# Kernel optimization log

Measured on AMD Instinct MI355X. Metric: run time of the kernel, lower is better.

The kernel has to match this reference:

```python
import jax, jax.numpy as jnp
import numpy as np

E = 8            # num experts
CAP_FACTOR = 1.5
K_THRESH = 0.8
BAL_ALPHA = 0.005
REG_ALPHA = 1e-6
BN_EPS = 1e-5
POOL = 16


def setup_inputs() -> dict:
    key = jax.random.key(0)
    ks = jax.random.split(key, 8)
    B, H, L, D = 128, 1024, 512, 1024
    return {
        "x": jax.random.normal(ks[0], (B, H, L), jnp.float32),
        "conv_w": jax.random.normal(ks[1], (64, H, 3), jnp.float32) / np.float32(np.sqrt(3 * H)),
        "conv_b": jnp.zeros((64,), jnp.float32),
        "bn_gamma": jnp.ones((64 * POOL,), jnp.float32),
        "bn_beta": jnp.zeros((64 * POOL,), jnp.float32),
        "fc1_w": jax.random.normal(ks[2], (128, 64 * POOL), jnp.float32) / np.float32(np.sqrt(64 * POOL)),
        "fc1_b": jnp.zeros((128,), jnp.float32),
        "fc2_w": jax.random.normal(ks[3], (E, 128), jnp.float32) / np.float32(np.sqrt(128)),
        "fc2_b": jnp.zeros((E,), jnp.float32),
        "exp_w": jax.random.normal(ks[4], (E, H, D), jnp.float32) / np.float32(np.sqrt(H)),
        "exp_b": jnp.zeros((E, D), jnp.float32),
    }


def _forward(x, conv_w, conv_b, bn_gamma, bn_beta, fc1_w, fc1_b, fc2_w, fc2_b, exp_w, exp_b):
    B, H, L = x.shape
    # ---- router: Conv1d(H->64,k=3,p=1) -> GELU -> AdaptiveAvgPool1d(16) -> Flatten -> BN -> FC -> GELU -> FC -> softmax
    h = jax.lax.conv_general_dilated(x, conv_w, (1,), ((1, 1),),
                                     dimension_numbers=("NCH", "OIH", "NCH"))
    h = jax.nn.gelu(h + conv_b[None, :, None], approximate=False)          # [B,64,L]; torch GELU is exact erf
    h = h.reshape(B, 64, POOL, L // POOL).mean(-1).reshape(B, 64 * POOL)   # adaptive avg pool (L%16==0) + flatten
    mu, var = h.mean(0), h.var(0)                                          # training-mode (Sync)BatchNorm: batch stats
    h = (h - mu) / jnp.sqrt(var + BN_EPS) * bn_gamma + bn_beta
    h = jax.nn.gelu(h @ fc1_w.T + fc1_b, approximate=False)
    rw = jax.nn.softmax(h @ fc2_w.T + fc2_b, axis=1)                       # [B,E]; expert dropout = identity (eval)
    # ---- dynamic k: smallest k s.t. cumsum of sorted probs > threshold; only max over batch is used
    topk_w, topk_idx = jax.lax.top_k(rw, E)                                # full descending sort
    cum = jnp.cumsum(topk_w, axis=1)
    over = cum > K_THRESH
    k_per = jnp.where(jnp.any(over, axis=1), jnp.argmax(over, axis=1) + 1, E)
    max_k = jnp.max(jnp.clip(k_per, 1, E))
    col_valid = jnp.arange(E)[None, :] < max_k                             # broadcast [B,E]; cols >= max_k unused
    assign = jnp.where(col_valid, topk_idx, -1)
    # ---- capacity enforcement: per expert keep the `capacity` highest-weight assignments, drop the rest (-1)
    capacity = max(1, int(B * CAP_FACTOR / E))
    flat_idx, flat_w = assign.reshape(-1), topk_w.reshape(-1)              # row-major [B*E], matches torch flatten

    def keep_for_expert(e):
        m = flat_idx == e
        order = jnp.argsort(-jnp.where(m, flat_w, -jnp.inf))               # descending within expert e
        ranks = jnp.zeros_like(order).at[order].set(jnp.arange(order.shape[0]))
        return m & (ranks < capacity)

    keep = jax.vmap(keep_for_expert)(jnp.arange(E))                        # [E, B*E]
    counts = keep.sum(axis=1).astype(jnp.float32)                          # == bincount of valid final indices
    final_idx = jnp.where(jnp.any(keep, axis=0), flat_idx, -1).reshape(B, E)
    # ---- experts: mean-pool over length, per-expert Linear(H->D); gather each sample's selected experts
    pooled = x.mean(axis=2)                                                # [B,H]
    y = jnp.einsum("bh,ehd->bed", pooled, exp_w) + exp_b[None]             # [B,E,D] all-expert outputs
    outputs = jnp.take_along_axis(y, jnp.clip(final_idx, 0)[..., None], axis=1)
    outputs = jnp.where(final_idx[..., None] >= 0, outputs, 0.0)           # dropped slots contribute zeros
    # ---- combine: softmax over the max_k slots; dropped (-1) slots enter softmax with logit 0, as in torch
    logits = jnp.where(col_valid, topk_w * (final_idx >= 0), -jnp.inf)
    norm_w = jax.nn.softmax(logits, axis=1)                                # [B,E]
    pooler = jnp.einsum("bkd,bk->bd", outputs, norm_w)                     # [B,D]
    # ---- losses / stats
    usage = rw.mean(0)
    reg = jnp.sum(exp_w * exp_w) + jnp.sum(exp_b * exp_b)                  # sum ||param||_2^2 over expert params
    added_loss = BAL_ALPHA * jnp.var(usage, ddof=1) + REG_ALPHA * reg      # torch.var is unbiased
    return pooler, added_loss, usage, counts


def reference(x, conv_w, conv_b, bn_gamma, bn_beta, fc1_w, fc1_b, fc2_w, fc2_b, exp_w, exp_b):
    return _forward(x, conv_w, conv_b, bn_gamma, bn_beta, fc1_w, fc1_b, fc2_w, fc2_b, exp_w, exp_b)
```

## Files before the change

### kernel.cpp

```cpp
#include <hip/hip_runtime.h>
#include <hip/hip_bf16.h>
#include <math.h>

#define NB 128
#define NH 1024
#define NL 512
#define OC 64
#define NE 8
#define ND 1024
#define CAPACITY 24

static const size_t WS_PART  = 0;
static const size_t WS_WSEP  = 1048576;
static const size_t WS_PXT   = 2097152;
static const size_t WS_HPOOL = 2228224;
static const size_t WS_SCALE = 2359296;
static const size_t WS_SHIFT = 2360320;
static const size_t WS_A1    = 2361344;
static const size_t WS_TKW   = 2377728;
static const size_t WS_TKI   = 2378752;
static const size_t WS_USAGE = 2379784;
static const size_t WS_VARU  = 2379792;
static const size_t WS_REG   = 2379793;
static const size_t WS_CNT   = 2379794;
static const size_t WS_WMAT  = 2380832;
static const size_t WS_RW    = 2381856;
static const size_t WS_KP    = 2382880;

typedef __attribute__((ext_vector_type(8))) short bf16x8;
typedef __attribute__((ext_vector_type(4))) float f32x4;

__device__ __forceinline__ float gelu_exact(float v) {
    return 0.5f * v * (1.0f + erff(v * 0.70710678118654752440f));
}

__device__ __forceinline__ unsigned short f2bf_rne(float f) {
    unsigned int u = __float_as_uint(f);
    unsigned int r = u + 0x7FFFu + ((u >> 16) & 1u);
    return (unsigned short)(r >> 16);
}
__device__ __forceinline__ float bf2f(unsigned short h) {
    return __uint_as_float(((unsigned int)h) << 16);
}

__device__ __forceinline__ unsigned cvtpk_bf16(float a, float b) {
    unsigned r;
    asm("v_cvt_pk_bf16_f32 %0, %1, %2" : "=v"(r) : "v"(a), "v"(b));
    return r;
}

__global__ __launch_bounds__(256) void k_wsplit(const float* __restrict__ cw, float* __restrict__ ws)
{
    if (blockIdx.x == 0 && threadIdx.x == 0) ws[WS_REG] = 0.0f;
    unsigned short* wsep = (unsigned short*)(ws + WS_WSEP);
    int i = blockIdx.x * 256 + threadIdx.x;
    float v = cw[i];
    int j = i % 3;
    int t = i / 3;
    int h = t & 1023;
    int o = t >> 10;
    int it = h >> 5;
    int h5 = h & 31;
    int e = h5 & 7;
    int lane = (o & 15) | ((h5 >> 3) << 4);
    int mt = (o >> 4) & 3;
    unsigned short hi = f2bf_rne(v);
    unsigned short lo = f2bf_rne(v - bf2f(hi));
    size_t base = ((size_t)((it * 3 + j) * 4 + mt) * 2) * 512 + lane * 8 + e;
    wsep[base] = hi;
    wsep[base + 512] = lo;
}

__device__ __forceinline__ void cvt_unit(unsigned int* X, int lq, int h4,
                                         const float4* v, float* sh)
{
    sh[0] = sh[1] = sh[2] = sh[3] = 0.f;
#pragma unroll
    for (int i = 0; i < 4; ++i) {
        float a0 = ((const float*)&v[0])[i];
        float a1 = ((const float*)&v[1])[i];
        float a2 = ((const float*)&v[2])[i];
        float a3 = ((const float*)&v[3])[i];
        sh[0] += a0; sh[1] += a1; sh[2] += a2; sh[3] += a3;
        unsigned h01 = cvtpk_bf16(a0, a1);
        unsigned h23 = cvtpk_bf16(a2, a3);
        float r0 = a0 - __uint_as_float(h01 << 16);
        float r1 = a1 - __uint_as_float(h01 & 0xFFFF0000u);
        float r2 = a2 - __uint_as_float(h23 << 16);
        float r3 = a3 - __uint_as_float(h23 & 0xFFFF0000u);
        unsigned l01 = cvtpk_bf16(r0, r1);
        unsigned l23 = cvtpk_bf16(r2, r3);
        int r = lq * 4 + i;
        unsigned int* dst = X + r * 34 + ((2 * h4) ^ ((r & 3) << 2));
        *(uint2*)dst = make_uint2(h01, h23);
        *(uint2*)(dst + 16) = make_uint2(l01, l23);
    }
}

__global__ __launch_bounds__(256, 2) void k_convmfma(const float* __restrict__ x,
                                                     const float* __restrict__ cb,
                                                     float* __restrict__ ws)
{
    __shared__ unsigned int Xb[2][136 * 34];
    __shared__ float xs2[3][128];
    __shared__ float scb[64];

    const int lc = blockIdx.x, b = blockIdx.y;
    const int l0 = lc * 128;
    const int tid = threadIdx.x;
    const int wv = tid >> 6, lane = tid & 63;
    const int h4 = tid & 7;
    const int lqi = 1 + (tid >> 3);
    const bool has_halo = (tid < 16);
    const int lqh = (tid < 8) ? 0 : 33;
    const bool halo_ok = (tid < 8) ? (lc > 0) : (lc < 3);

    const unsigned short* wsg = (const unsigned short*)(ws + WS_WSEP);
    const float* xbase = x + (size_t)b * (NH * NL);
    float* poolp = ws + WS_PART + ((size_t)(lc * 128 + b)) * 1024;

    if (tid < 64) scb[tid] = cb[tid];

    f32x4 acc[4][2];
#pragma unroll
    for (int mt = 0; mt < 4; ++mt)
#pragma unroll
        for (int nt = 0; nt < 2; ++nt) acc[mt][nt] = (f32x4){0.f, 0.f, 0.f, 0.f};

    float4 xA[4], hA[4], xB[4], hB[4];

    auto xload = [&](int itL, float4* xc, float4* hc) {
        const int hn = itL * 32;
        const float* p = xbase + (size_t)(hn + h4 * 4) * NL + (l0 - 4 + lqi * 4);
#pragma unroll
        for (int jj = 0; jj < 4; ++jj) xc[jj] = *(const float4*)(p + jj * NL);
        if (has_halo) {
            int gl = l0 - 4 + lqh * 4;
#pragma unroll
            for (int jj = 0; jj < 4; ++jj)
                hc[jj] = halo_ok ? *(const float4*)(xbase + (size_t)(hn + h4 * 4 + jj) * NL + gl)
                                 : make_float4(0.f, 0.f, 0.f, 0.f);
        }
    };

    auto body = [&](int it, float4* xc, float4* hc) {
        unsigned int* Xw = Xb[it & 1];
        bf16x8 Ar[3][4][2];
        {
            const unsigned short* abase = wsg + (size_t)it * 12288 + lane * 8;
#pragma unroll
            for (int j = 0; j < 3; ++j)
#pragma unroll
                for (int mt = 0; mt < 4; ++mt) {
                    Ar[j][mt][0] = *(const bf16x8*)(abase + (size_t)(j * 8 + mt * 2) * 512);
                    Ar[j][mt][1] = *(const bf16x8*)(abase + (size_t)(j * 8 + mt * 2 + 1) * 512);
                }
        }
        {
            float sh[4];
            cvt_unit(Xw, lqi, h4, xc, sh);
#pragma unroll
            for (int jj = 0; jj < 4; ++jj) {
                float s = sh[jj];
                s += __shfl_xor(s, 8, 64);
                s += __shfl_xor(s, 16, 64);
                s += __shfl_xor(s, 32, 64);
                if ((lane >> 3) == 0) xs2[it % 3][wv * 32 + h4 * 4 + jj] = s;
            }
            if (has_halo) { float d[4]; cvt_unit(Xw, lqh, h4, hc, d); }
        }
        __syncthreads();
        if (it > 0 && tid < 32) {
            const float* S = xs2[(it - 1) % 3];
            poolp[(it - 1) * 32 + tid] = S[tid] + S[32 + tid] + S[64 + tid] + S[96 + tid];
        }
        if (it < 30) xload(it + 2, xc, hc);
        const int g4 = (lane >> 4) << 2;
#pragma unroll
        for (int j = 0; j < 3; ++j) {
            bf16x8 Bh[2], Bl[2];
#pragma unroll
            for (int nt = 0; nt < 2; ++nt) {
                int rx = 3 + j + wv * 32 + nt * 16 + (lane & 15);
                const unsigned int* bp = Xw + rx * 34 + (g4 ^ ((rx & 3) << 2));
                Bh[nt] = *(const bf16x8*)bp;
                Bl[nt] = *(const bf16x8*)(bp + 16);
            }
#pragma unroll
            for (int mt = 0; mt < 4; ++mt)
#pragma unroll
                for (int nt = 0; nt < 2; ++nt) {
                    acc[mt][nt] = __builtin_amdgcn_mfma_f32_16x16x32_bf16(Ar[j][mt][0], Bh[nt], acc[mt][nt], 0, 0, 0);
                    acc[mt][nt] = __builtin_amdgcn_mfma_f32_16x16x32_bf16(Ar[j][mt][0], Bl[nt], acc[mt][nt], 0, 0, 0);
                    acc[mt][nt] = __builtin_amdgcn_mfma_f32_16x16x32_bf16(Ar[j][mt][1], Bh[nt], acc[mt][nt], 0, 0, 0);
                }
        }
    };

    xload(0, xA, hA);
    xload(1, xB, hB);

    for (int it2 = 0; it2 < 32; it2 += 2) {
        body(it2, xA, hA);
        body(it2 + 1, xB, hB);
    }
    if (tid < 32) {
        const float* S = xs2[31 % 3];
        poolp[31 * 32 + tid] = S[tid] + S[32 + tid] + S[64 + tid] + S[96 + tid];
    }

    {
        const int g = lane >> 4, cidx = lane & 15;
#pragma unroll
        for (int mt = 0; mt < 4; ++mt) {
            float s[4];
#pragma unroll
            for (int r = 0; r < 4; ++r) {
                int o = mt * 16 + g * 4 + r;
                float bo = scb[o];
                s[r] = gelu_exact(acc[mt][0][r] + bo) + gelu_exact(acc[mt][1][r] + bo);
            }
#pragma unroll
            for (int m = 1; m < 16; m <<= 1) {
#pragma unroll
                for (int r = 0; r < 4; ++r) s[r] += __shfl_xor(s[r], m, 64);
            }
            if (cidx == 0) {
#pragma unroll
                for (int r = 0; r < 4; ++r) {
                    int o = mt * 16 + g * 4 + r;
                    ws[WS_HPOOL + (size_t)b * 1024 + o * 16 + lc * 4 + wv] = s[r] * (1.0f / 32.0f);
                }
            }
        }
    }
}

__global__ __launch_bounds__(256) void k_mid(const float* __restrict__ g,
                                             const float* __restrict__ bet,
                                             float* __restrict__ ws)
{
    int bx = blockIdx.x;
    if (bx < 512) {
        int id = bx * 256 + threadIdx.x;
        int b = id >> 10, h = id & 1023;
        float s = 0.0f;
#pragma unroll
        for (int lcc = 0; lcc < 4; lcc++) s += ws[WS_PART + ((size_t)(lcc * 128 + b)) * 1024 + h];
        ws[WS_PXT + (size_t)h * 128 + b] = s * (1.0f / 512.0f);
    } else {
        int f = (bx - 512) * 256 + threadIdx.x;
        const float* hp = ws + WS_HPOOL;
        float s = 0.0f;
        for (int b = 0; b < 128; b++) s += hp[(size_t)b * 1024 + f];
        float mu = s * (1.0f / 128.0f);
        float v = 0.0f;
        for (int b = 0; b < 128; b++) { float d = hp[(size_t)b * 1024 + f] - mu; v += d * d; }
        float var = v * (1.0f / 128.0f);
        float sc = g[f] / sqrtf(var + 1e-5f);
        ws[WS_SCALE + f] = sc;
        ws[WS_SHIFT + f] = bet[f] - mu * sc;
    }
}

__global__ __launch_bounds__(256) void k_fused(const float* __restrict__ w1,
                                               const float* __restrict__ b1,
                                               const float* __restrict__ w2,
                                               const float* __restrict__ b2,
                                               const float* __restrict__ ew,
                                               const float* __restrict__ eb,
                                               float* __restrict__ ws)
{
    __shared__ float smem[6400];
    const int bx = blockIdx.x;
    const int tid = threadIdx.x;

    if (bx < 256) {
        float* a_s = smem;
        float* b_s = smem + 4096;
        float* red2 = smem + 6144;
        const int e = bx >> 5, dt = (bx >> 1) & 15, ks = bx & 1;
        const int tb = tid >> 3, td = tid & 7;
        float acc[4][8];
#pragma unroll
        for (int i = 0; i < 4; i++)
#pragma unroll
            for (int j = 0; j < 8; j++) acc[i][j] = 0.0f;
        float ssq = 0.0f;

        const float* pxt = ws + WS_PXT;
        for (int kt = 0; kt < 512; kt += 32) {
            __syncthreads();
            for (int idx = tid; idx < 4096; idx += 256) {
                int kk = idx >> 7, bb = idx & 127;
                a_s[kk * 128 + bb] = pxt[(size_t)(ks * 512 + kt + kk) * 128 + bb];
            }
            for (int idx = tid; idx < 2048; idx += 256) {
                int kk = idx >> 6, d = idx & 63;
                float v = ew[(size_t)e * 1048576 + (size_t)(ks * 512 + kt + kk) * 1024 + dt * 64 + d];
                b_s[kk * 64 + d] = v;
                ssq += v * v;
            }
            __syncthreads();
#pragma unroll 4
            for (int kk = 0; kk < 32; kk++) {
                float4 av = *(const float4*)&a_s[kk * 128 + tb * 4];
                float4 b0 = *(const float4*)&b_s[kk * 64 + td * 8];
                float4 b1v = *(const float4*)&b_s[kk * 64 + td * 8 + 4];
                float aa[4] = {av.x, av.y, av.z, av.w};
                float bb4[8] = {b0.x, b0.y, b0.z, b0.w, b1v.x, b1v.y, b1v.z, b1v.w};
#pragma unroll
                for (int i = 0; i < 4; i++)
#pragma unroll
                    for (int j = 0; j < 8; j++) acc[i][j] = fmaf(aa[i], bb4[j], acc[i][j]);
            }
        }
        float* outp = ws + WS_PART + ((size_t)(ks * 8 + e) * 128) * 1024 + dt * 64;
#pragma unroll
        for (int i = 0; i < 4; i++) {
            int bb = tb * 4 + i;
            *(float4*)(outp + (size_t)bb * 1024 + td * 8) =
                make_float4(acc[i][0], acc[i][1], acc[i][2], acc[i][3]);
            *(float4*)(outp + (size_t)bb * 1024 + td * 8 + 4) =
                make_float4(acc[i][4], acc[i][5], acc[i][6], acc[i][7]);
        }
        if (bx == 0)
            for (int i = tid; i < 8192; i += 256) { float v = eb[i]; ssq += v * v; }
        red2[tid] = ssq;
        __syncthreads();
        for (int off = 128; off > 0; off >>= 1) {
            if (tid < off) red2[tid] += red2[tid + off];
            __syncthreads();
        }
        if (tid == 0) atomicAdd(ws + WS_REG, red2[0]);
    } else {
        float* hb  = smem;
        float* red = smem + 1024;
        float* ha  = smem + 1280;
        float* w2s = smem + 1408;
        float* lg  = smem + 2432;
        const int b = bx - 256;
        const float* hp = ws + WS_HPOOL + (size_t)b * 1024;
        for (int k = tid; k < 1024; k += 256)
            hb[k] = hp[k] * ws[WS_SCALE + k] + ws[WS_SHIFT + k];
        for (int i = tid; i < 1024; i += 256) w2s[i] = w2[i];
        __syncthreads();
        int o = tid & 127, kh = tid >> 7;
        const float4* wrp = (const float4*)(w1 + (size_t)o * 1024 + kh * 512);
        const float* hx = hb + kh * 512;
        float acc = 0.0f;
#pragma unroll 4
        for (int k = 0; k < 128; k++) {
            float4 w = wrp[k];
            acc = fmaf(hx[4 * k], w.x, acc);     acc = fmaf(hx[4 * k + 1], w.y, acc);
            acc = fmaf(hx[4 * k + 2], w.z, acc); acc = fmaf(hx[4 * k + 3], w.w, acc);
        }
        red[tid] = acc;
        __syncthreads();
        if (tid < 128)
            ha[tid] = gelu_exact(red[tid] + red[tid + 128] + b1[tid]);
        __syncthreads();
        if (tid < 8) {
            float a2 = b2[tid];
            for (int k = 0; k < 128; k++) a2 = fmaf(ha[k], w2s[tid * 128 + k], a2);
            lg[tid] = a2;
        }
        __syncthreads();
        if (tid == 0) {
            float rw[8];
            float m = -1e30f;
#pragma unroll
            for (int e = 0; e < 8; e++) m = fmaxf(m, lg[e]);
            float s = 0.0f;
#pragma unroll
            for (int e = 0; e < 8; e++) { rw[e] = expf(lg[e] - m); s += rw[e]; }
            float inv = 1.0f / s;
#pragma unroll
            for (int e = 0; e < 8; e++) { rw[e] *= inv; ws[WS_RW + b * 8 + e] = rw[e]; }
            float tw[8]; int ti[8]; unsigned used = 0;
#pragma unroll
            for (int r = 0; r < 8; r++) {
                float bv = -1e30f; int bi = 0;
#pragma unroll
                for (int e = 0; e < 8; e++) {
                    bool take = !((used >> e) & 1u) && (rw[e] > bv);
                    bv = take ? rw[e] : bv;
                    bi = take ? e : bi;
                }
                used |= (1u << bi);
                tw[r] = bv; ti[r] = bi;
            }
            float cum = 0.0f; int kp = 8;
#pragma unroll
            for (int r = 0; r < 8; r++) {
                cum += tw[r];
                if (cum > 0.8f) { kp = r + 1; break; }
            }
#pragma unroll
            for (int r = 0; r < 8; r++) {
                ws[WS_TKW + b * 8 + r] = tw[r];
                ((int*)ws)[WS_TKI + b * 8 + r] = ti[r];
            }
            ((int*)ws)[WS_KP + b] = kp;
        }
    }
}

__global__ __launch_bounds__(128) void k_route(float* __restrict__ ws)
{
    __shared__ float tkw_s[1024];
    __shared__ int   tki_s[1024];
    __shared__ int   keep_s[1024];
    __shared__ float wv_s[128];
    __shared__ int   sv_s[128];
    __shared__ float usg[8];
    __shared__ int   cnt_s[8];
    __shared__ int   mk;

    const int tid = threadIdx.x;
    const int b = tid;
    if (tid == 0) mk = 0;
    if (tid < 8) cnt_s[tid] = 0;
    __syncthreads();
    atomicMax(&mk, ((const int*)ws)[WS_KP + b]);
#pragma unroll
    for (int r = 0; r < 8; r++) {
        tkw_s[b * 8 + r] = ws[WS_TKW + b * 8 + r];
        tki_s[b * 8 + r] = ((const int*)ws)[WS_TKI + b * 8 + r];
    }
    __syncthreads();
    const int maxk = mk;

    if (tid < 8) {
        float s2 = 0.0f;
        for (int bb = 0; bb < 128; bb++) s2 += ws[WS_RW + bb * 8 + tid];
        float u = s2 * (1.0f / 128.0f);
        usg[tid] = u;
        ws[WS_USAGE + tid] = u;
    }
    __syncthreads();
    if (tid == 0) {
        float mu = 0.0f;
#pragma unroll
        for (int e = 0; e < 8; e++) mu += usg[e];
        mu *= (1.0f / 8.0f);
        float v = 0.0f;
#pragma unroll
        for (int e = 0; e < 8; e++) { float d = usg[e] - mu; v += d * d; }
        ws[WS_VARU] = v * (1.0f / 7.0f);
    }

    for (int e = 0; e < 8; ++e) {
        float myw = 0.0f; int mys = -1;
        for (int k = 0; k < maxk; k++)
            if (tki_s[b * 8 + k] == e) { myw = tkw_s[b * 8 + k]; mys = b * 8 + k; }
        wv_s[b] = myw; sv_s[b] = mys;
        __syncthreads();
        if (mys >= 0) {
            int rank = 0;
            for (int b2 = 0; b2 < 128; b2++) {
                int s2 = sv_s[b2];
                if (s2 >= 0) {
                    float w2v = wv_s[b2];
                    if (w2v > myw || (w2v == myw && s2 < mys)) rank++;
                }
            }
            int kept = (rank < CAPACITY) ? 1 : 0;
            keep_s[mys] = kept;
            if (kept) atomicAdd(&cnt_s[e], 1);
        }
        __syncthreads();
    }
    if (tid < 8) ws[WS_CNT + tid] = (float)cnt_s[tid];

    float lv[8]; int kept[8]; int idx[8];
#pragma unroll
    for (int k = 0; k < 8; k++) {
        if (k < maxk) {
            kept[k] = keep_s[b * 8 + k];
            idx[k] = tki_s[b * 8 + k];
            lv[k] = kept[k] ? tkw_s[b * 8 + k] : 0.0f;
        } else { kept[k] = 0; idx[k] = -1; lv[k] = -1e30f; }
    }
    float mx = -1e30f;
#pragma unroll
    for (int k = 0; k < 8; k++) if (k < maxk) mx = fmaxf(mx, lv[k]);
    float s3 = 0.0f; float ev[8];
#pragma unroll
    for (int k = 0; k < 8; k++) { ev[k] = (k < maxk) ? expf(lv[k] - mx) : 0.0f; s3 += ev[k]; }
    float inv3 = 1.0f / s3;
    float Wr[8] = {0, 0, 0, 0, 0, 0, 0, 0};
#pragma unroll
    for (int k = 0; k < 8; k++) {
        if (kept[k]) {
            float v = ev[k] * inv3;
#pragma unroll
            for (int e = 0; e < 8; e++) Wr[e] += (idx[k] == e) ? v : 0.0f;
        }
    }
#pragma unroll
    for (int e = 0; e < 8; e++) ws[WS_WMAT + b * 8 + e] = Wr[e];
}

__global__ __launch_bounds__(256) void k_final(const float* __restrict__ eb,
                                               const float* __restrict__ ws,
                                               float* __restrict__ out)
{
    int id = blockIdx.x * 256 + threadIdx.x;
    int b = id >> 10, d = id & 1023;
    const float* wm = ws + WS_WMAT + b * 8;
    const float* Y = ws + WS_PART;
    float s = 0.0f;
#pragma unroll
    for (int e = 0; e < 8; e++) {
        float y = Y[((size_t)e * 128 + b) * 1024 + d]
                + Y[((size_t)(8 + e) * 128 + b) * 1024 + d]
                + eb[(size_t)e * 1024 + d];
        s += wm[e] * y;
    }
    out[id] = s;
    if (blockIdx.x == 0) {
        int t = threadIdx.x;
        if (t == 0) out[131072] = 0.005f * ws[WS_VARU] + 1e-6f * ws[WS_REG];
        else if (t >= 1 && t < 9)  out[131072 + t] = ws[WS_USAGE + t - 1];
        else if (t >= 9 && t < 17) out[131072 + t] = ws[WS_CNT + t - 9];
    }
}

extern "C" void kernel_launch(void* const* d_in, const int* in_sizes, int n_in,
                              void* d_out, int out_size, void* d_ws, size_t ws_size,
                              hipStream_t stream)
{
    const float* x   = (const float*)d_in[0];
    const float* cw  = (const float*)d_in[1];
    const float* cb  = (const float*)d_in[2];
    const float* bng = (const float*)d_in[3];
    const float* bnb = (const float*)d_in[4];
    const float* f1w = (const float*)d_in[5];
    const float* f1b = (const float*)d_in[6];
    const float* f2w = (const float*)d_in[7];
    const float* f2b = (const float*)d_in[8];
    const float* ew  = (const float*)d_in[9];
    const float* eb  = (const float*)d_in[10];
    float* ws  = (float*)d_ws;
    float* out = (float*)d_out;

    k_wsplit  <<<768, 256, 0, stream>>>(cw, ws);
    k_convmfma<<<dim3(4, 128), 256, 0, stream>>>(x, cb, ws);
    k_mid     <<<516, 256, 0, stream>>>(bng, bnb, ws);
    k_fused   <<<384, 256, 0, stream>>>(f1w, f1b, f2w, f2b, ew, eb, ws);
    k_route   <<<1, 128, 0, stream>>>(ws);
    k_final   <<<512, 256, 0, stream>>>(eb, ws, out);
}
```

Measured before the change: 316.0 us.

## Repartition conv MFMA by output-channel per wave, vectorize wsplit and final, finer expert tiles

The conv kernel now gives each wave one 16-channel M tile across all eight 16-column N tiles, instead of all four M tiles across two N tiles. That cuts per-wave A-fragment register loads from 24 to 6 and lowers register pressure, at the cost of more LDS B reads. The weight-split kernel now writes packed 16-byte vectors per thread, the expert GEMM uses 32-wide D tiles over twice as many blocks for better occupancy, and the final combine kernel is vectorized with float4. Together these change work partitioning and memory access patterns across several kernels.

```diff
diff --git a/kernel.cpp b/kernel.cpp
--- a/kernel.cpp
+++ b/kernel.cpp
@@ -16,7 +16,6 @@
 static const size_t WS_HPOOL = 2228224;
 static const size_t WS_SCALE = 2359296;
 static const size_t WS_SHIFT = 2360320;
-static const size_t WS_A1    = 2361344;
 static const size_t WS_TKW   = 2377728;
 static const size_t WS_TKI   = 2378752;
 static const size_t WS_USAGE = 2379784;
@@ -54,21 +53,22 @@
     if (blockIdx.x == 0 && threadIdx.x == 0) ws[WS_REG] = 0.0f;
     unsigned short* wsep = (unsigned short*)(ws + WS_WSEP);
     int i = blockIdx.x * 256 + threadIdx.x;
-    float v = cw[i];
-    int j = i % 3;
-    int t = i / 3;
-    int h = t & 1023;
-    int o = t >> 10;
-    int it = h >> 5;
-    int h5 = h & 31;
-    int e = h5 & 7;
-    int lane = (o & 15) | ((h5 >> 3) << 4);
-    int mt = (o >> 4) & 3;
-    unsigned short hi = f2bf_rne(v);
-    unsigned short lo = f2bf_rne(v - bf2f(hi));
-    size_t base = ((size_t)((it * 3 + j) * 4 + mt) * 2) * 512 + lane * 8 + e;
-    wsep[base] = hi;
-    wsep[base + 512] = lo;
+    int lane = i & 63;
+    int split = (i >> 6) & 1;
+    int mt = (i >> 7) & 3;
+    int rest = i >> 9;
+    int j = rest % 3;
+    int it = rest / 3;
+    int o = mt * 16 + (lane & 15);
+    int hb = it * 32 + ((lane >> 4) << 3);
+    unsigned short v8[8];
+#pragma unroll
+    for (int e = 0; e < 8; ++e) {
+        float v = cw[((size_t)o * 1024 + hb + e) * 3 + j];
+        unsigned short hi = f2bf_rne(v);
+        v8[e] = split ? f2bf_rne(v - bf2f(hi)) : hi;
+    }
+    *(uint4*)(wsep + ((size_t)((it * 3 + j) * 4 + mt) * 2 + split) * 512 + lane * 8) = *(uint4*)v8;
 }
 
 __device__ __forceinline__ void cvt_unit(unsigned int* X, int lq, int h4,
@@ -121,11 +121,9 @@
 
     if (tid < 64) scb[tid] = cb[tid];
 
-    f32x4 acc[4][2];
-#pragma unroll
-    for (int mt = 0; mt < 4; ++mt)
-#pragma unroll
-        for (int nt = 0; nt < 2; ++nt) acc[mt][nt] = (f32x4){0.f, 0.f, 0.f, 0.f};
+    f32x4 acc[8];
+#pragma unroll
+    for (int nt = 0; nt < 8; ++nt) acc[nt] = (f32x4){0.f, 0.f, 0.f, 0.f};
 
     float4 xA[4], hA[4], xB[4], hB[4];
 
@@ -145,16 +143,14 @@
 
     auto body = [&](int it, float4* xc, float4* hc) {
         unsigned int* Xw = Xb[it & 1];
-        bf16x8 Ar[3][4][2];
+        bf16x8 Ah[3], Al[3];
         {
             const unsigned short* abase = wsg + (size_t)it * 12288 + lane * 8;
 #pragma unroll
-            for (int j = 0; j < 3; ++j)
-#pragma unroll
-                for (int mt = 0; mt < 4; ++mt) {
-                    Ar[j][mt][0] = *(const bf16x8*)(abase + (size_t)(j * 8 + mt * 2) * 512);
-                    Ar[j][mt][1] = *(const bf16x8*)(abase + (size_t)(j * 8 + mt * 2 + 1) * 512);
-                }
+            for (int j = 0; j < 3; ++j) {
+                Ah[j] = *(const bf16x8*)(abase + (size_t)((j * 4 + wv) * 2) * 512);
+                Al[j] = *(const bf16x8*)(abase + (size_t)((j * 4 + wv) * 2 + 1) * 512);
+            }
         }
         {
             float sh[4];
@@ -178,22 +174,16 @@
         const int g4 = (lane >> 4) << 2;
 #pragma unroll
         for (int j = 0; j < 3; ++j) {
-            bf16x8 Bh[2], Bl[2];
-#pragma unroll
-            for (int nt = 0; nt < 2; ++nt) {
-                int rx = 3 + j + wv * 32 + nt * 16 + (lane & 15);
+#pragma unroll
+            for (int nt = 0; nt < 8; ++nt) {
+                int rx = 3 + j + nt * 16 + (lane & 15);
                 const unsigned int* bp = Xw + rx * 34 + (g4 ^ ((rx & 3) << 2));
-                Bh[nt] = *(const bf16x8*)bp;
-                Bl[nt] = *(const bf16x8*)(bp + 16);
-            }
-#pragma unroll
-            for (int mt = 0; mt < 4; ++mt)
-#pragma unroll
-                for (int nt = 0; nt < 2; ++nt) {
-                    acc[mt][nt] = __builtin_amdgcn_mfma_f32_16x16x32_bf16(Ar[j][mt][0], Bh[nt], acc[mt][nt], 0, 0, 0);
-                    acc[mt][nt] = __builtin_amdgcn_mfma_f32_16x16x32_bf16(Ar[j][mt][0], Bl[nt], acc[mt][nt], 0, 0, 0);
-                    acc[mt][nt] = __builtin_amdgcn_mfma_f32_16x16x32_bf16(Ar[j][mt][1], Bh[nt], acc[mt][nt], 0, 0, 0);
-                }
+                bf16x8 Bh = *(const bf16x8*)bp;
+                bf16x8 Bl = *(const bf16x8*)(bp + 16);
+                acc[nt] = __builtin_amdgcn_mfma_f32_16x16x32_bf16(Ah[j], Bh, acc[nt], 0, 0, 0);
+                acc[nt] = __builtin_amdgcn_mfma_f32_16x16x32_bf16(Ah[j], Bl, acc[nt], 0, 0, 0);
+                acc[nt] = __builtin_amdgcn_mfma_f32_16x16x32_bf16(Al[j], Bh, acc[nt], 0, 0, 0);
+            }
         }
     };
 
@@ -212,13 +202,13 @@
     {
         const int g = lane >> 4, cidx = lane & 15;
 #pragma unroll
-        for (int mt = 0; mt < 4; ++mt) {
+        for (int np = 0; np < 4; ++np) {
             float s[4];
 #pragma unroll
             for (int r = 0; r < 4; ++r) {
-                int o = mt * 16 + g * 4 + r;
+                int o = wv * 16 + g * 4 + r;
                 float bo = scb[o];
-                s[r] = gelu_exact(acc[mt][0][r] + bo) + gelu_exact(acc[mt][1][r] + bo);
+                s[r] = gelu_exact(acc[2 * np][r] + bo) + gelu_exact(acc[2 * np + 1][r] + bo);
             }
 #pragma unroll
             for (int m = 1; m < 16; m <<= 1) {
@@ -228,8 +218,8 @@
             if (cidx == 0) {
 #pragma unroll
                 for (int r = 0; r < 4; ++r) {
-                    int o = mt * 16 + g * 4 + r;
-                    ws[WS_HPOOL + (size_t)b * 1024 + o * 16 + lc * 4 + wv] = s[r] * (1.0f / 32.0f);
+                    int o = wv * 16 + g * 4 + r;
+                    ws[WS_HPOOL + (size_t)b * 1024 + o * 16 + lc * 4 + np] = s[r] * (1.0f / 32.0f);
                 }
             }
         }
@@ -271,21 +261,21 @@
                                                const float* __restrict__ eb,
                                                float* __restrict__ ws)
 {
-    __shared__ float smem[6400];
+    __shared__ float smem[5376];
     const int bx = blockIdx.x;
     const int tid = threadIdx.x;
 
-    if (bx < 256) {
+    if (bx < 512) {
         float* a_s = smem;
         float* b_s = smem + 4096;
-        float* red2 = smem + 6144;
-        const int e = bx >> 5, dt = (bx >> 1) & 15, ks = bx & 1;
+        float* red2 = smem + 5120;
+        const int e = bx >> 6, dt = (bx >> 1) & 31, ks = bx & 1;
         const int tb = tid >> 3, td = tid & 7;
-        float acc[4][8];
+        float acc[4][4];
 #pragma unroll
         for (int i = 0; i < 4; i++)
 #pragma unroll
-            for (int j = 0; j < 8; j++) acc[i][j] = 0.0f;
+            for (int j = 0; j < 4; j++) acc[i][j] = 0.0f;
         float ssq = 0.0f;
 
         const float* pxt = ws + WS_PXT;
@@ -295,34 +285,31 @@
                 int kk = idx >> 7, bb = idx & 127;
                 a_s[kk * 128 + bb] = pxt[(size_t)(ks * 512 + kt + kk) * 128 + bb];
             }
-            for (int idx = tid; idx < 2048; idx += 256) {
-                int kk = idx >> 6, d = idx & 63;
-                float v = ew[(size_t)e * 1048576 + (size_t)(ks * 512 + kt + kk) * 1024 + dt * 64 + d];
-                b_s[kk * 64 + d] = v;
+            for (int idx = tid; idx < 1024; idx += 256) {
+                int kk = idx >> 5, d = idx & 31;
+                float v = ew[(size_t)e * 1048576 + (size_t)(ks * 512 + kt + kk) * 1024 + dt * 32 + d];
+                b_s[kk * 32 + d] = v;
                 ssq += v * v;
             }
             __syncthreads();
 #pragma unroll 4
             for (int kk = 0; kk < 32; kk++) {
                 float4 av = *(const float4*)&a_s[kk * 128 + tb * 4];
-                float4 b0 = *(const float4*)&b_s[kk * 64 + td * 8];
-                float4 b1v = *(const float4*)&b_s[kk * 64 + td * 8 + 4];
+                float4 bv = *(const float4*)&b_s[kk * 32 + td * 4];
                 float aa[4] = {av.x, av.y, av.z, av.w};
-                float bb4[8] = {b0.x, b0.y, b0.z, b0.w, b1v.x, b1v.y, b1v.z, b1v.w};
+                float bb4[4] = {bv.x, bv.y, bv.z, bv.w};
 #pragma unroll
                 for (int i = 0; i < 4; i++)
 #pragma unroll
-                    for (int j = 0; j < 8; j++) acc[i][j] = fmaf(aa[i], bb4[j], acc[i][j]);
-            }
-        }
-        float* outp = ws + WS_PART + ((size_t)(ks * 8 + e) * 128) * 1024 + dt * 64;
+                    for (int j = 0; j < 4; j++) acc[i][j] = fmaf(aa[i], bb4[j], acc[i][j]);
+            }
+        }
+        float* outp = ws + WS_PART + ((size_t)(ks * 8 + e) * 128) * 1024 + dt * 32;
 #pragma unroll
         for (int i = 0; i < 4; i++) {
             int bb = tb * 4 + i;
-            *(float4*)(outp + (size_t)bb * 1024 + td * 8) =
+            *(float4*)(outp + (size_t)bb * 1024 + td * 4) =
                 make_float4(acc[i][0], acc[i][1], acc[i][2], acc[i][3]);
-            *(float4*)(outp + (size_t)bb * 1024 + td * 8 + 4) =
-                make_float4(acc[i][4], acc[i][5], acc[i][6], acc[i][7]);
         }
         if (bx == 0)
             for (int i = tid; i < 8192; i += 256) { float v = eb[i]; ssq += v * v; }
@@ -339,7 +326,7 @@
         float* ha  = smem + 1280;
         float* w2s = smem + 1408;
         float* lg  = smem + 2432;
-        const int b = bx - 256;
+        const int b = bx - 512;
         const float* hp = ws + WS_HPOOL + (size_t)b * 1024;
         for (int k = tid; k < 1024; k += 256)
             hb[k] = hp[k] * ws[WS_SCALE + k] + ws[WS_SHIFT + k];
@@ -507,18 +494,22 @@
                                                float* __restrict__ out)
 {
     int id = blockIdx.x * 256 + threadIdx.x;
-    int b = id >> 10, d = id & 1023;
+    int b = id >> 8, dq = id & 255;
     const float* wm = ws + WS_WMAT + b * 8;
     const float* Y = ws + WS_PART;
-    float s = 0.0f;
+    float4 s = make_float4(0.f, 0.f, 0.f, 0.f);
 #pragma unroll
     for (int e = 0; e < 8; e++) {
-        float y = Y[((size_t)e * 128 + b) * 1024 + d]
-                + Y[((size_t)(8 + e) * 128 + b) * 1024 + d]
-                + eb[(size_t)e * 1024 + d];
-        s += wm[e] * y;
-    }
-    out[id] = s;
+        float4 y0 = *(const float4*)(Y + ((size_t)e * 128 + b) * 1024 + dq * 4);
+        float4 y1 = *(const float4*)(Y + ((size_t)(8 + e) * 128 + b) * 1024 + dq * 4);
+        float4 bb = *(const float4*)(eb + (size_t)e * 1024 + dq * 4);
+        float w = wm[e];
+        s.x += w * (y0.x + y1.x + bb.x);
+        s.y += w * (y0.y + y1.y + bb.y);
+        s.z += w * (y0.z + y1.z + bb.z);
+        s.w += w * (y0.w + y1.w + bb.w);
+    }
+    *(float4*)(out + (size_t)b * 1024 + dq * 4) = s;
     if (blockIdx.x == 0) {
         int t = threadIdx.x;
         if (t == 0) out[131072] = 0.005f * ws[WS_VARU] + 1e-6f * ws[WS_REG];
@@ -545,10 +536,10 @@
     float* ws  = (float*)d_ws;
     float* out = (float*)d_out;
 
-    k_wsplit  <<<768, 256, 0, stream>>>(cw, ws);
+    k_wsplit  <<<192, 256, 0, stream>>>(cw, ws);
     k_convmfma<<<dim3(4, 128), 256, 0, stream>>>(x, cb, ws);
     k_mid     <<<516, 256, 0, stream>>>(bng, bnb, ws);
-    k_fused   <<<384, 256, 0, stream>>>(f1w, f1b, f2w, f2b, ew, eb, ws);
+    k_fused   <<<640, 256, 0, stream>>>(f1w, f1b, f2w, f2b, ew, eb, ws);
     k_route   <<<1, 128, 0, stream>>>(ws);
-    k_final   <<<512, 256, 0, stream>>>(eb, ws, out);
-}
+    k_final   <<<128, 256, 0, stream>>>(eb, ws, out);
+}
```

Result: slower. 549.5 us (+73.9%).
